# Optimization experiments

Measured on AMD Instinct MI355X. Metric: run time of the kernel, lower is better.

The kernel has to match this reference:

```python
import jax, jax.numpy as jnp
import numpy as np

EMBED = 768
HEADS = 12
HEAD_DIM = EMBED // HEADS
HIDDEN = int(EMBED * 4.0)
EPS = 1e-5


def setup_inputs() -> dict:
    key = jax.random.key(0)
    ks = jax.random.split(key, 12)
    s = 0.02
    return {
        "x": jax.random.normal(ks[0], (8, 1024, EMBED), dtype=jnp.float32),
        # norm1 / norm2 (LayerNorm affine params)
        "g1": jnp.ones((EMBED,), jnp.float32),
        "b1": jnp.zeros((EMBED,), jnp.float32),
        "g2": jnp.ones((EMBED,), jnp.float32),
        "b2": jnp.zeros((EMBED,), jnp.float32),
        # attention weights (stored [in, out]; qkv_bias=False)
        "w_qkv": jax.random.normal(ks[1], (EMBED, 3 * EMBED), jnp.float32) * s,
        "w_proj": jax.random.normal(ks[2], (EMBED, EMBED), jnp.float32) * s,
        "b_proj": jnp.zeros((EMBED,), jnp.float32),
        # MLP weights
        "w_fc1": jax.random.normal(ks[3], (EMBED, HIDDEN), jnp.float32) * s,
        "b_fc1": jnp.zeros((HIDDEN,), jnp.float32),
        "w_fc2": jax.random.normal(ks[4], (HIDDEN, EMBED), jnp.float32) * s,
        "b_fc2": jnp.zeros((EMBED,), jnp.float32),
    }


def _layernorm(x, g, b):
    mu = jnp.mean(x, axis=-1, keepdims=True)
    var = jnp.var(x, axis=-1, keepdims=True)
    return (x - mu) * jax.lax.rsqrt(var + EPS) * g + b


def reference(x, g1, b1, g2, b2, w_qkv, w_proj, b_proj, w_fc1, b_fc1, w_fc2, b_fc2):
    B, N, C = x.shape
    scaling = HEAD_DIM ** (-0.5)

    # --- attention branch ---
    h = _layernorm(x, g1, b1)
    qkv = (h @ w_qkv).reshape(B, N, 3, HEADS, HEAD_DIM)
    q, k, v = qkv[:, :, 0], qkv[:, :, 1], qkv[:, :, 2]  # [B, N, H, D]
    attn = jnp.einsum("bnhd,bmhd->bhnm", q, k) * scaling  # full NxN scores
    attn = jax.nn.softmax(attn, axis=-1)
    out = jnp.einsum("bhnm,bmhd->bnhd", attn, v).reshape(B, N, C)
    out = out @ w_proj + b_proj
    x = x + out

    # --- MLP branch ---
    h = _layernorm(x, g2, b2)
    h = jax.nn.gelu(h @ w_fc1 + b_fc1, approximate=False)
    h = h @ w_fc2 + b_fc2
    return x + h
```

## Files before the change

kernel.cpp:

```cpp
#include <hip/hip_runtime.h>
#include <hip/hip_bf16.h>
#include <math.h>

#define EMBED 768
#define HEADS 12
#define HEAD_DIM 64
#define HIDDEN 3072
#define SEQ 1024
#define BATCH 8
#define TOKENS (SEQ*BATCH)

typedef unsigned short u16;
typedef __attribute__((ext_vector_type(8))) short bf16x8;
typedef __attribute__((ext_vector_type(4))) float floatx4;
typedef __attribute__((ext_vector_type(4))) u16 u16x4;
typedef __attribute__((ext_vector_type(2))) u16 u16x2;

__device__ __forceinline__ u16 f2bf(float f){
    union { float f; unsigned u; } v; v.f = f;
    unsigned r = v.u + 0x7fffu + ((v.u >> 16) & 1u);
    return (u16)(r >> 16);
}

__device__ __forceinline__ unsigned cvt_pk_bf16(float lo, float hi){
    unsigned r;
    asm("v_cvt_pk_bf16_f32 %0, %1, %2" : "=v"(r) : "v"(lo), "v"(hi));
    return r;
}

__device__ __forceinline__ void gload16(const void* g, void* l){
    __builtin_amdgcn_global_load_lds((const __attribute__((address_space(1))) void*)g,
                                     (__attribute__((address_space(3))) void*)l, 16, 0, 0);
}

__device__ __forceinline__ float gelu_fast(float x){
    float t = 1.5957691216f * (x + 0.044715f * x * x * x);
    return x / (1.0f + __expf(-t));
}

__global__ __launch_bounds__(256) void prep_kernel(const float* __restrict__ w0, const float* __restrict__ w1,
                                   const float* __restrict__ w2, const float* __restrict__ w3,
                                   u16* __restrict__ o0, u16* __restrict__ o1,
                                   u16* __restrict__ o2, u16* __restrict__ o3,
                                   const float* __restrict__ x, const float* __restrict__ g,
                                   const float* __restrict__ bln, u16* __restrict__ lnout){
    int bb = blockIdx.x;
    int tid = threadIdx.x;
    if(bb >= 6912){
        int row  = (bb - 6912) * 4 + (tid >> 6);
        int lane = tid & 63;
        const float4* xr = (const float4*)(x + (size_t)row * EMBED);
        float4 v[3];
        float s = 0.f;
        #pragma unroll
        for(int i=0;i<3;i++){
            v[i] = xr[i*64 + lane];
            s += v[i].x + v[i].y + v[i].z + v[i].w;
        }
        #pragma unroll
        for(int o=32;o>0;o>>=1) s += __shfl_xor(s, o);
        float mu = s * (1.0f/EMBED);
        float s2 = 0.f;
        #pragma unroll
        for(int i=0;i<3;i++){
            float dx = v[i].x-mu, dy = v[i].y-mu, dz = v[i].z-mu, dw = v[i].w-mu;
            s2 += dx*dx + dy*dy + dz*dz + dw*dw;
        }
        #pragma unroll
        for(int o=32;o>0;o>>=1) s2 += __shfl_xor(s2, o);
        float rstd = rsqrtf(s2*(1.0f/EMBED) + 1e-5f);
        u16* orow = lnout + (size_t)row * EMBED;
        const float4* g4 = (const float4*)g;
        const float4* b4 = (const float4*)bln;
        #pragma unroll
        for(int i=0;i<3;i++){
            int c4 = i*64 + lane;
            float4 gv = g4[c4], bv = b4[c4];
            u16x4 pk;
            pk.x = f2bf((v[i].x-mu)*rstd*gv.x + bv.x);
            pk.y = f2bf((v[i].y-mu)*rstd*gv.y + bv.y);
            pk.z = f2bf((v[i].z-mu)*rstd*gv.z + bv.z);
            pk.w = f2bf((v[i].w-mu)*rstd*gv.w + bv.w);
            *(u16x4*)(orow + c4*4) = pk;
        }
        return;
    }
    const float* W; u16* Wt; int K, N, bx, by;
    if(bb < 1728)      { int l = bb;        W=w0; Wt=o0; K=768;  N=2304; bx=l%72; by=l/72; }
    else if(bb < 2304) { int l = bb-1728;   W=w1; Wt=o1; K=768;  N=768;  bx=l%24; by=l/24; }
    else if(bb < 4608) { int l = bb-2304;   W=w2; Wt=o2; K=768;  N=3072; bx=l%96; by=l/96; }
    else               { int l = bb-4608;   W=w3; Wt=o3; K=3072; N=768;  bx=l%24; by=l/24; }

    __shared__ float tile[32][33];
    int n0 = bx * 32, k0 = by * 32;
    int tx = tid & 31, ty = tid >> 5;
    #pragma unroll
    for(int i=0;i<32;i+=8) tile[ty+i][tx] = W[(size_t)(k0+ty+i)*N + n0+tx];
    __syncthreads();
    int kp = (tid & 15)*2, nn = tid >> 4;
    #pragma unroll
    for(int p=0;p<2;p++){
        int n = nn + p*16;
        u16x2 w2v;
        w2v.x = f2bf(tile[kp  ][n]);
        w2v.y = f2bf(tile[kp+1][n]);
        *(u16x2*)(Wt + (size_t)(n0+n)*K + k0 + kp) = w2v;
    }
}

__global__ __launch_bounds__(256) void ln_kernel(const float* __restrict__ x, const float* __restrict__ g,
                                                 const float* __restrict__ b, u16* __restrict__ out){
    int row  = blockIdx.x * 4 + (threadIdx.x >> 6);
    int lane = threadIdx.x & 63;
    const float4* xr = (const float4*)(x + (size_t)row * EMBED);
    float4 v[3];
    float s = 0.f;
    #pragma unroll
    for(int i=0;i<3;i++){
        v[i] = xr[i*64 + lane];
        s += v[i].x + v[i].y + v[i].z + v[i].w;
    }
    #pragma unroll
    for(int o=32;o>0;o>>=1) s += __shfl_xor(s, o);
    float mu = s * (1.0f/EMBED);
    float s2 = 0.f;
    #pragma unroll
    for(int i=0;i<3;i++){
        float dx = v[i].x-mu, dy = v[i].y-mu, dz = v[i].z-mu, dw = v[i].w-mu;
        s2 += dx*dx + dy*dy + dz*dz + dw*dw;
    }
    #pragma unroll
    for(int o=32;o>0;o>>=1) s2 += __shfl_xor(s2, o);
    float rstd = rsqrtf(s2*(1.0f/EMBED) + 1e-5f);
    u16* orow = out + (size_t)row * EMBED;
    const float4* g4 = (const float4*)g;
    const float4* b4 = (const float4*)b;
    #pragma unroll
    for(int i=0;i<3;i++){
        int c4 = i*64 + lane;
        float4 gv = g4[c4], bv = b4[c4];
        u16x4 pk;
        pk.x = f2bf((v[i].x-mu)*rstd*gv.x + bv.x);
        pk.y = f2bf((v[i].y-mu)*rstd*gv.y + bv.y);
        pk.z = f2bf((v[i].z-mu)*rstd*gv.z + bv.z);
        pk.w = f2bf((v[i].w-mu)*rstd*gv.w + bv.w);
        *(u16x4*)(orow + c4*4) = pk;
    }
}

template<int EPI>
__global__ __launch_bounds__(512,4) void gemm_wide(const u16* __restrict__ A, const u16* __restrict__ Bt,
        void* __restrict__ Cout, const float* __restrict__ bias, const float* __restrict__ res,
        u16* __restrict__ vt, int M, int N, int K, int ldc){
    __shared__ __align__(16) u16 As[128*64];
    __shared__ __align__(16) u16 Bs[2*256*64];
    int tid  = threadIdx.x;
    int wave = tid >> 6, lane = tid & 63;
    int quad = lane >> 4, lm = lane & 15;
    int wm = (wave >> 2) * 64;
    int wn = (wave & 3) * 64;

    int gx = gridDim.x;
    int bid = blockIdx.y * gx + blockIdx.x;
    int nwg = gx * gridDim.y;
    int cpx = nwg >> 3;
    int swz = (bid & 7) * cpx + (bid >> 3);
    int m0 = (swz / gx) * 128, n0 = (swz % gx) * 256;

    floatx4 acc[4][4];
    #pragma unroll
    for(int i=0;i<4;i++)
        #pragma unroll
        for(int j=0;j<4;j++) acc[i][j] = (floatx4){0.f,0.f,0.f,0.f};

    int srow = tid >> 3;
    int scol = ((tid & 7) ^ (srow & 7)) * 8;
    const u16* aP[2];
    const u16* bP[4];
    #pragma unroll
    for(int p=0;p<2;p++) aP[p] = A  + (size_t)(m0 + p*64 + srow) * K + scol;
    #pragma unroll
    for(int p=0;p<4;p++) bP[p] = Bt + (size_t)(n0 + p*64 + srow) * K + scol;

    int nt = K / 64;
    #pragma unroll
    for(int p=0;p<4;p++) gload16(bP[p], Bs + p*4096 + tid*8);

    for(int t=0; t<nt; ++t){
        int cur = t & 1, nxt = cur ^ 1;
        size_t k0 = (size_t)t * 64;
        #pragma unroll
        for(int p=0;p<2;p++) gload16(aP[p] + k0, As + p*4096 + tid*8);
        if(t+1 < nt){
            #pragma unroll
            for(int p=0;p<4;p++) gload16(bP[p] + k0 + 64, Bs + nxt*16384 + p*4096 + tid*8);
            asm volatile("s_waitcnt vmcnt(4)" ::: "memory");
        } else {
            asm volatile("s_waitcnt vmcnt(0)" ::: "memory");
        }
        __builtin_amdgcn_s_barrier();
        const u16* Bc = Bs + cur*16384;
        #pragma unroll
        for(int ks=0;ks<2;ks++){
            int slotoff = (((ks*4+quad) ^ (lm&7)) << 3);
            bf16x8 af[4], bfr[4];
            #pragma unroll
            for(int i=0;i<4;i++)
                af[i]  = *(const bf16x8*)(As + (wm + i*16 + lm)*64 + slotoff);
            #pragma unroll
            for(int i=0;i<4;i++)
                bfr[i] = *(const bf16x8*)(Bc + (wn + i*16 + lm)*64 + slotoff);
            #pragma unroll
            for(int mf=0;mf<4;mf++)
                #pragma unroll
                for(int nf=0;nf<4;nf++)
                    acc[mf][nf] = __builtin_amdgcn_mfma_f32_16x16x32_bf16(af[mf], bfr[nf], acc[mf][nf], 0, 0, 0);
        }
        __builtin_amdgcn_s_barrier();
    }

    if(EPI == 3 && n0 >= 1536){
        #pragma unroll
        for(int nf=0;nf<4;nf++){
            int col = n0 + wn + nf*16 + lm;
            int hh = (col - 1536) >> 6;
            int d  = col & 63;
            #pragma unroll
            for(int mf=0;mf<4;mf++){
                int row0 = m0 + wm + mf*16 + quad*4;
                int bb  = row0 >> 10;
                int key = row0 & 1023;
                u16x4 pk;
                #pragma unroll
                for(int r=0;r<4;r++) pk[r] = f2bf(acc[mf][nf][r]);
                *(u16x4*)(vt + ((size_t)(bb*HEADS+hh)*64 + d)*SEQ + key) = pk;
            }
        }
        return;
    }

    float bvv[4];
    #pragma unroll
    for(int nf=0;nf<4;nf++) bvv[nf] = bias ? bias[n0 + wn + nf*16 + lm] : 0.f;
    #pragma unroll
    for(int mf=0;mf<4;mf++){
        int row0 = m0 + wm + mf*16 + quad*4;
        #pragma unroll
        for(int r=0;r<4;r++){
            size_t rowoff = (size_t)(row0 + r) * ldc;
            #pragma unroll
            for(int nf=0;nf<4;nf++){
                int col = n0 + wn + nf*16 + lm;
                float v = acc[mf][nf][r] + bvv[nf];
                if(EPI == 1) v = gelu_fast(v);
                if(EPI == 3 && col < 768) v *= 0.18033688011112186f;
                ((u16*)Cout)[rowoff + col] = f2bf(v);
            }
        }
    }
}

template<int EPI, int BM>
__global__ __launch_bounds__(256) void gemm_bt(const u16* __restrict__ A, const u16* __restrict__ Bt,
        void* __restrict__ Cout, const float* __restrict__ bias, const float* __restrict__ res,
        u16* __restrict__ vt, int M, int N, int K, int ldc){
    constexpr int MF = BM/32;
    __shared__ __align__(16) u16 As[BM*64];
    __shared__ __align__(16) u16 Bs[2*128*64];
    int tid  = threadIdx.x;
    int wave = tid >> 6, lane = tid & 63;
    int quad = lane >> 4, lm = lane & 15;

    int gx = gridDim.x;
    int bid = blockIdx.y * gx + blockIdx.x;
    int nwg = gx * gridDim.y;
    int cpx = nwg >> 3;
    int swz = (bid & 7) * cpx + (bid >> 3);
    int m0 = (swz / gx) * BM, n0 = (swz % gx) * 128;

    int wm = (wave & 1) * (BM/2);
    int wn = (wave >> 1) * 64;

    floatx4 acc[MF][4];
    #pragma unroll
    for(int i=0;i<MF;i++)
        #pragma unroll
        for(int j=0;j<4;j++) acc[i][j] = (floatx4){0.f,0.f,0.f,0.f};

    int srow = tid >> 3;
    int scol = ((tid & 7) ^ (srow & 7)) * 8;
    const u16* aP[MF];
    const u16* bP[4];
    #pragma unroll
    for(int p=0;p<MF;p++) aP[p] = A  + (size_t)(m0 + p*32 + srow) * K + scol;
    #pragma unroll
    for(int p=0;p<4;p++)  bP[p] = Bt + (size_t)(n0 + p*32 + srow) * K + scol;

    int nt = K / 64;
    #pragma unroll
    for(int p=0;p<4;p++) gload16(bP[p], Bs + p*2048 + tid*8);

    for(int t=0; t<nt; ++t){
        int cur = t & 1, nxt = cur ^ 1;
        size_t k0 = (size_t)t * 64;
        #pragma unroll
        for(int p=0;p<MF;p++) gload16(aP[p] + k0, As + p*2048 + tid*8);
        if(t+1 < nt){
            #pragma unroll
            for(int p=0;p<4;p++) gload16(bP[p] + k0 + 64, Bs + nxt*8192 + p*2048 + tid*8);
            asm volatile("s_waitcnt vmcnt(4)" ::: "memory");
        } else {
            asm volatile("s_waitcnt vmcnt(0)" ::: "memory");
        }
        __builtin_amdgcn_s_barrier();
        const u16* Bc = Bs + cur*8192;
        #pragma unroll
        for(int ks=0;ks<2;ks++){
            int slotoff = (((ks*4+quad) ^ (lm&7)) << 3);
            bf16x8 af[MF], bfr[4];
            #pragma unroll
            for(int i=0;i<MF;i++)
                af[i]  = *(const bf16x8*)(As + (wm + i*16 + lm)*64 + slotoff);
            #pragma unroll
            for(int i=0;i<4;i++)
                bfr[i] = *(const bf16x8*)(Bc + (wn + i*16 + lm)*64 + slotoff);
            #pragma unroll
            for(int mf=0;mf<MF;mf++)
                #pragma unroll
                for(int nf=0;nf<4;nf++)
                    acc[mf][nf] = __builtin_amdgcn_mfma_f32_16x16x32_bf16(af[mf], bfr[nf], acc[mf][nf], 0, 0, 0);
        }
        __builtin_amdgcn_s_barrier();
    }

    float bvv[4];
    #pragma unroll
    for(int nf=0;nf<4;nf++) bvv[nf] = bias ? bias[n0 + wn + nf*16 + lm] : 0.f;
    #pragma unroll
    for(int mf=0;mf<MF;mf++){
        int row0 = m0 + wm + mf*16 + quad*4;
        #pragma unroll
        for(int r=0;r<4;r++){
            size_t rowoff = (size_t)(row0 + r) * ldc;
            #pragma unroll
            for(int nf=0;nf<4;nf++){
                int col = n0 + wn + nf*16 + lm;
                float v = acc[mf][nf][r] + bvv[nf];
                if(EPI == 2){
                    ((float*)Cout)[rowoff + col] = v + res[rowoff + col];
                } else {
                    ((u16*)Cout)[rowoff + col] = f2bf(v);
                }
            }
        }
    }
}

__global__ __launch_bounds__(256) void attn_kernel(const u16* __restrict__ qk, const u16* __restrict__ vt,
                                                   u16* __restrict__ out){
    int bid = blockIdx.x;
    int hb = bid % 96;
    int qt = bid / 96;
    int h = hb % HEADS, b = hb / HEADS;
    int tid = threadIdx.x;
    int wave = tid >> 6, lane = tid & 63;
    int quad = lane >> 4, lm = lane & 15;

    __shared__ __align__(16) u16 Ks[2*64*64];
    __shared__ __align__(16) u16 Vs[2*64*64];
    __shared__ __align__(16) u16 P[4*32*64];

    const u16* qbase = qk + (size_t)b * SEQ * 1536;
    const u16* vbase = vt + (size_t)(b*HEADS + h) * 64 * SEQ;
    u16* Pw = P + wave*2048;

    int q0 = qt*128 + wave*32;
    bf16x8 qf[2][2];
    #pragma unroll
    for(int qi=0;qi<2;qi++){
        const u16* qp = qbase + (size_t)(q0 + qi*16 + lm)*1536 + h*64;
        qf[qi][0] = *(const bf16x8*)(qp + quad*8);
        qf[qi][1] = *(const bf16x8*)(qp + 32 + quad*8);
    }

    float l_i[2] = {0.f, 0.f};
    floatx4 o_acc[2][4];
    #pragma unroll
    for(int qi=0;qi<2;qi++)
        #pragma unroll
        for(int nf=0;nf<4;nf++) o_acc[qi][nf] = (floatx4){0.f,0.f,0.f,0.f};

    int sr = lane >> 3;
    int sp = lane & 7;

    auto stage = [&](int kt, int buf){
        #pragma unroll
        for(int i=0;i<2;i++){
            int rr = wave*16 + i*8 + sr;
            int sw = (sp ^ (rr & 7)) * 8;
            gload16(qbase + (size_t)(kt*64 + rr)*1536 + 768 + h*64 + sw,
                    Ks + buf*4096 + (wave*16 + i*8)*64 + lane*8);
            gload16(vbase + (size_t)rr*SEQ + kt*64 + sw,
                    Vs + buf*4096 + (wave*16 + i*8)*64 + lane*8);
        }
    };

    stage(0, 0);
    __syncthreads();

    int cur = 0;
    for(int kt=0; kt<16; kt++){
        if(kt < 15) stage(kt+1, cur^1);
        const u16* Ksb = Ks + cur*4096;
        const u16* Vsb = Vs + cur*4096;

        floatx4 s[4][2];
        #pragma unroll
        for(int kf=0;kf<4;kf++){
            int krow = kf*16 + lm;
            bf16x8 k0 = *(const bf16x8*)(Ksb + krow*64 + ((quad     ^ (lm&7))*8));
            bf16x8 k1 = *(const bf16x8*)(Ksb + krow*64 + (((4+quad) ^ (lm&7))*8));
            #pragma unroll
            for(int qi=0;qi<2;qi++){
                floatx4 t = (floatx4){0.f,0.f,0.f,0.f};
                t = __builtin_amdgcn_mfma_f32_16x16x32_bf16(k0, qf[qi][0], t, 0, 0, 0);
                t = __builtin_amdgcn_mfma_f32_16x16x32_bf16(k1, qf[qi][1], t, 0, 0, 0);
                s[kf][qi] = t;
            }
        }

        #pragma unroll
        for(int qi=0;qi<2;qi++){
            float part = 0.f;
            #pragma unroll
            for(int kf=0;kf<4;kf++){
                #pragma unroll
                for(int r=0;r<4;r++){
                    float e = exp2f(s[kf][qi][r]);
                    s[kf][qi][r] = e;
                    part += e;
                }
            }
            l_i[qi] += part;
            #pragma unroll
            for(int kf=0;kf<4;kf++){
                uint2 pk2;
                pk2.x = cvt_pk_bf16(s[kf][qi][0], s[kf][qi][1]);
                pk2.y = cvt_pk_bf16(s[kf][qi][2], s[kf][qi][3]);
                int c  = kf*4 + quad;
                int cp = c ^ (2*(lm & 7));
                *(uint2*)(Pw + (qi*16 + lm)*64 + cp*4) = pk2;
            }
        }

        #pragma unroll
        for(int ks=0;ks<2;ks++){
            bf16x8 vf[4];
            #pragma unroll
            for(int nf=0;nf<4;nf++)
                vf[nf] = *(const bf16x8*)(Vsb + (nf*16+lm)*64 + (((ks*4+quad) ^ (lm&7))*8));
            #pragma unroll
            for(int qi=0;qi<2;qi++){
                int cr = (ks*8 + 2*quad) ^ (2*(lm & 7));
                bf16x8 pa = *(const bf16x8*)(Pw + (qi*16 + lm)*64 + cr*4);
                #pragma unroll
                for(int nf=0;nf<4;nf++)
                    o_acc[qi][nf] = __builtin_amdgcn_mfma_f32_16x16x32_bf16(pa, vf[nf], o_acc[qi][nf], 0, 0, 0);
            }
        }
        if(kt < 15) __syncthreads();
        cur ^= 1;
    }

    #pragma unroll
    for(int qi=0;qi<2;qi++){
        float lf = l_i[qi];
        lf += __shfl_xor(lf, 16);
        lf += __shfl_xor(lf, 32);
        float rl[4];
        #pragma unroll
        for(int r=0;r<4;r++) rl[r] = 1.0f / __shfl(lf, quad*4 + r);
        int token = b*SEQ + qt*128 + wave*32 + qi*16 + quad*4;
        #pragma unroll
        for(int r=0;r<4;r++){
            size_t rowoff = (size_t)(token + r)*EMBED + h*64;
            #pragma unroll
            for(int nf=0;nf<4;nf++){
                out[rowoff + nf*16 + lm] = f2bf(o_acc[qi][nf][r] * rl[r]);
            }
        }
    }
}

extern "C" void kernel_launch(void* const* d_in, const int* in_sizes, int n_in,
                              void* d_out, int out_size, void* d_ws, size_t ws_size,
                              hipStream_t stream) {
    const float* x      = (const float*)d_in[0];
    const float* g1     = (const float*)d_in[1];
    const float* b1     = (const float*)d_in[2];
    const float* g2     = (const float*)d_in[3];
    const float* b2     = (const float*)d_in[4];
    const float* w_qkv  = (const float*)d_in[5];
    const float* w_proj = (const float*)d_in[6];
    const float* b_proj = (const float*)d_in[7];
    const float* w_fc1  = (const float*)d_in[8];
    const float* b_fc1  = (const float*)d_in[9];
    const float* w_fc2  = (const float*)d_in[10];
    const float* b_fc2  = (const float*)d_in[11];
    float* out = (float*)d_out;

    char* ws = (char*)d_ws;
    u16*   wqkv_t  = (u16*)  (ws + 0);
    u16*   wproj_t = (u16*)  (ws + 3538944);
    u16*   wfc1_t  = (u16*)  (ws + 4718592);
    u16*   wfc2_t  = (u16*)  (ws + 9437184);
    float* x1      = (float*)(ws + 14155776);
    u16*   hbuf    = (u16*)  (ws + 39321600);
    u16*   qkbuf   = (u16*)  (ws + 51904512);
    u16*   vtbuf   = (u16*)  (ws + 77070336);
    u16*   attn_o  = (u16*)  (ws + 89653248);
    u16*   fc1_o   = qkbuf;
    u16*   h2      = hbuf;

    prep_kernel<<<8960, 256, 0, stream>>>(w_qkv, w_proj, w_fc1, w_fc2,
                                          wqkv_t, wproj_t, wfc1_t, wfc2_t,
                                          x, g1, b1, hbuf);

    gemm_wide<3><<<dim3(2304/256, TOKENS/128), 512, 0, stream>>>(hbuf, wqkv_t, qkbuf, nullptr, nullptr, vtbuf, TOKENS, 2304, 768, 1536);

    attn_kernel<<<768, 256, 0, stream>>>(qkbuf, vtbuf, attn_o);

    gemm_bt<2,64><<<dim3( 768/128, TOKENS/64), 256, 0, stream>>>(attn_o, wproj_t, x1, b_proj, x, nullptr, TOKENS, 768, 768, 768);

    ln_kernel<<<TOKENS/4, 256, 0, stream>>>(x1, g2, b2, h2);

    gemm_wide<1><<<dim3(3072/256, TOKENS/128), 512, 0, stream>>>(h2, wfc1_t, fc1_o, b_fc1, nullptr, nullptr, TOKENS, 3072, 768, 3072);

    gemm_bt<2,64><<<dim3( 768/128, TOKENS/64), 256, 0, stream>>>(fc1_o, wfc2_t, out, b_fc2, x1, nullptr, TOKENS, 768, 3072, 768);
}
```

Baseline: 323.8 us.

## Halve GEMM K-tile to 32 and double-buffer both A and B in LDS

Both GEMM kernels move from a 64-wide K tile, where only B was double-buffered, to a 32-wide K tile with A and B both double-buffered. Each thread now issues one 16-byte load per operand slice, and the LDS swizzle is reworked for 32-element rows. The aim is to overlap all global loads with MFMA work, cut LDS footprint and raise occupancy (launch bounds are adjusted). The cost is twice as many barriers and loop iterations per K, each doing less MFMA work.

Result: slower. 363.8 us (+12.4%).

```diff
diff --git a/kernel.cpp b/kernel.cpp
--- a/kernel.cpp
+++ b/kernel.cpp
@@ -149,11 +149,13 @@
 }
 
 template<int EPI>
-__global__ __launch_bounds__(512,4) void gemm_wide(const u16* __restrict__ A, const u16* __restrict__ Bt,
+__global__ __launch_bounds__(512,2) void gemm_wide(const u16* __restrict__ A, const u16* __restrict__ Bt,
         void* __restrict__ Cout, const float* __restrict__ bias, const float* __restrict__ res,
         u16* __restrict__ vt, int M, int N, int K, int ldc){
-    __shared__ __align__(16) u16 As[128*64];
-    __shared__ __align__(16) u16 Bs[2*256*64];
+    constexpr int ASZ = 128*32;
+    constexpr int BSZ = 256*32;
+    __shared__ __align__(16) u16 As[2*ASZ];
+    __shared__ __align__(16) u16 Bs[2*BSZ];
     int tid  = threadIdx.x;
     int wave = tid >> 6, lane = tid & 63;
     int quad = lane >> 4, lm = lane & 15;
@@ -173,49 +175,45 @@
         #pragma unroll
         for(int j=0;j<4;j++) acc[i][j] = (floatx4){0.f,0.f,0.f,0.f};
 
-    int srow = tid >> 3;
-    int scol = ((tid & 7) ^ (srow & 7)) * 8;
-    const u16* aP[2];
-    const u16* bP[4];
-    #pragma unroll
-    for(int p=0;p<2;p++) aP[p] = A  + (size_t)(m0 + p*64 + srow) * K + scol;
-    #pragma unroll
-    for(int p=0;p<4;p++) bP[p] = Bt + (size_t)(n0 + p*64 + srow) * K + scol;
-
-    int nt = K / 64;
-    #pragma unroll
-    for(int p=0;p<4;p++) gload16(bP[p], Bs + p*4096 + tid*8);
+    int srow = tid >> 2;
+    int scol = ((tid & 3) ^ ((tid >> 4) & 3)) * 8;
+    const u16* aP  = A  + (size_t)(m0 + srow) * K + scol;
+    const u16* bP0 = Bt + (size_t)(n0 + srow) * K + scol;
+    const u16* bP1 = Bt + (size_t)(n0 + 128 + srow) * K + scol;
+    int cr8 = (quad ^ (lm >> 2)) * 8;
+
+    int nt = K / 32;
+
+    gload16(aP,  As + tid*8);
+    gload16(bP0, Bs + tid*8);
+    gload16(bP1, Bs + 4096 + tid*8);
 
     for(int t=0; t<nt; ++t){
         int cur = t & 1, nxt = cur ^ 1;
-        size_t k0 = (size_t)t * 64;
-        #pragma unroll
-        for(int p=0;p<2;p++) gload16(aP[p] + k0, As + p*4096 + tid*8);
         if(t+1 < nt){
-            #pragma unroll
-            for(int p=0;p<4;p++) gload16(bP[p] + k0 + 64, Bs + nxt*16384 + p*4096 + tid*8);
-            asm volatile("s_waitcnt vmcnt(4)" ::: "memory");
+            size_t ko = (size_t)(t+1) * 32;
+            gload16(aP  + ko, As + nxt*ASZ + tid*8);
+            gload16(bP0 + ko, Bs + nxt*BSZ + tid*8);
+            gload16(bP1 + ko, Bs + nxt*BSZ + 4096 + tid*8);
+            asm volatile("s_waitcnt vmcnt(3)" ::: "memory");
         } else {
             asm volatile("s_waitcnt vmcnt(0)" ::: "memory");
         }
         __builtin_amdgcn_s_barrier();
-        const u16* Bc = Bs + cur*16384;
-        #pragma unroll
-        for(int ks=0;ks<2;ks++){
-            int slotoff = (((ks*4+quad) ^ (lm&7)) << 3);
-            bf16x8 af[4], bfr[4];
-            #pragma unroll
-            for(int i=0;i<4;i++)
-                af[i]  = *(const bf16x8*)(As + (wm + i*16 + lm)*64 + slotoff);
-            #pragma unroll
-            for(int i=0;i<4;i++)
-                bfr[i] = *(const bf16x8*)(Bc + (wn + i*16 + lm)*64 + slotoff);
-            #pragma unroll
-            for(int mf=0;mf<4;mf++)
-                #pragma unroll
-                for(int nf=0;nf<4;nf++)
-                    acc[mf][nf] = __builtin_amdgcn_mfma_f32_16x16x32_bf16(af[mf], bfr[nf], acc[mf][nf], 0, 0, 0);
-        }
+        const u16* Ac = As + cur*ASZ;
+        const u16* Bc = Bs + cur*BSZ;
+        bf16x8 af[4], bfr[4];
+        #pragma unroll
+        for(int mf=0;mf<4;mf++)
+            af[mf]  = *(const bf16x8*)(Ac + (wm + mf*16 + lm)*32 + cr8);
+        #pragma unroll
+        for(int nf=0;nf<4;nf++)
+            bfr[nf] = *(const bf16x8*)(Bc + (wn + nf*16 + lm)*32 + cr8);
+        #pragma unroll
+        for(int mf=0;mf<4;mf++)
+            #pragma unroll
+            for(int nf=0;nf<4;nf++)
+                acc[mf][nf] = __builtin_amdgcn_mfma_f32_16x16x32_bf16(af[mf], bfr[nf], acc[mf][nf], 0, 0, 0);
         __builtin_amdgcn_s_barrier();
     }
 
@@ -260,13 +258,14 @@
     }
 }
 
-template<int EPI, int BM>
-__global__ __launch_bounds__(256) void gemm_bt(const u16* __restrict__ A, const u16* __restrict__ Bt,
+template<int EPI>
+__global__ __launch_bounds__(256,4) void gemm_nar(const u16* __restrict__ A, const u16* __restrict__ Bt,
         void* __restrict__ Cout, const float* __restrict__ bias, const float* __restrict__ res,
         u16* __restrict__ vt, int M, int N, int K, int ldc){
-    constexpr int MF = BM/32;
-    __shared__ __align__(16) u16 As[BM*64];
-    __shared__ __align__(16) u16 Bs[2*128*64];
+    constexpr int ASZ = 64*32;
+    constexpr int BSZ = 128*32;
+    __shared__ __align__(16) u16 As[2*ASZ];
+    __shared__ __align__(16) u16 Bs[2*BSZ];
     int tid  = threadIdx.x;
     int wave = tid >> 6, lane = tid & 63;
     int quad = lane >> 4, lm = lane & 15;
@@ -276,60 +275,56 @@
     int nwg = gx * gridDim.y;
     int cpx = nwg >> 3;
     int swz = (bid & 7) * cpx + (bid >> 3);
-    int m0 = (swz / gx) * BM, n0 = (swz % gx) * 128;
-
-    int wm = (wave & 1) * (BM/2);
+    int m0 = (swz / gx) * 64, n0 = (swz % gx) * 128;
+
+    int wm = (wave & 1) * 32;
     int wn = (wave >> 1) * 64;
 
-    floatx4 acc[MF][4];
-    #pragma unroll
-    for(int i=0;i<MF;i++)
+    floatx4 acc[2][4];
+    #pragma unroll
+    for(int i=0;i<2;i++)
         #pragma unroll
         for(int j=0;j<4;j++) acc[i][j] = (floatx4){0.f,0.f,0.f,0.f};
 
-    int srow = tid >> 3;
-    int scol = ((tid & 7) ^ (srow & 7)) * 8;
-    const u16* aP[MF];
-    const u16* bP[4];
-    #pragma unroll
-    for(int p=0;p<MF;p++) aP[p] = A  + (size_t)(m0 + p*32 + srow) * K + scol;
-    #pragma unroll
-    for(int p=0;p<4;p++)  bP[p] = Bt + (size_t)(n0 + p*32 + srow) * K + scol;
-
-    int nt = K / 64;
-    #pragma unroll
-    for(int p=0;p<4;p++) gload16(bP[p], Bs + p*2048 + tid*8);
+    int srow = tid >> 2;
+    int scol = ((tid & 3) ^ ((tid >> 4) & 3)) * 8;
+    const u16* aP  = A  + (size_t)(m0 + srow) * K + scol;
+    const u16* bP0 = Bt + (size_t)(n0 + srow) * K + scol;
+    const u16* bP1 = Bt + (size_t)(n0 + 64 + srow) * K + scol;
+    int cr8 = (quad ^ (lm >> 2)) * 8;
+
+    int nt = K / 32;
+
+    gload16(aP,  As + tid*8);
+    gload16(bP0, Bs + tid*8);
+    gload16(bP1, Bs + 2048 + tid*8);
 
     for(int t=0; t<nt; ++t){
         int cur = t & 1, nxt = cur ^ 1;
-        size_t k0 = (size_t)t * 64;
-        #pragma unroll
-        for(int p=0;p<MF;p++) gload16(aP[p] + k0, As + p*2048 + tid*8);
         if(t+1 < nt){
-            #pragma unroll
-            for(int p=0;p<4;p++) gload16(bP[p] + k0 + 64, Bs + nxt*8192 + p*2048 + tid*8);
-            asm volatile("s_waitcnt vmcnt(4)" ::: "memory");
+            size_t ko = (size_t)(t+1) * 32;
+            gload16(aP  + ko, As + nxt*ASZ + tid*8);
+            gload16(bP0 + ko, Bs + nxt*BSZ + tid*8);
+            gload16(bP1 + ko, Bs + nxt*BSZ + 2048 + tid*8);
+            asm volatile("s_waitcnt vmcnt(3)" ::: "memory");
         } else {
             asm volatile("s_waitcnt vmcnt(0)" ::: "memory");
         }
         __builtin_amdgcn_s_barrier();
-        const u16* Bc = Bs + cur*8192;
-        #pragma unroll
-        for(int ks=0;ks<2;ks++){
-            int slotoff = (((ks*4+quad) ^ (lm&7)) << 3);
-            bf16x8 af[MF], bfr[4];
-            #pragma unroll
-            for(int i=0;i<MF;i++)
-                af[i]  = *(const bf16x8*)(As + (wm + i*16 + lm)*64 + slotoff);
-            #pragma unroll
-            for(int i=0;i<4;i++)
-                bfr[i] = *(const bf16x8*)(Bc + (wn + i*16 + lm)*64 + slotoff);
-            #pragma unroll
-            for(int mf=0;mf<MF;mf++)
-                #pragma unroll
-                for(int nf=0;nf<4;nf++)
-                    acc[mf][nf] = __builtin_amdgcn_mfma_f32_16x16x32_bf16(af[mf], bfr[nf], acc[mf][nf], 0, 0, 0);
-        }
+        const u16* Ac = As + cur*ASZ;
+        const u16* Bc = Bs + cur*BSZ;
+        bf16x8 af[2], bfr[4];
+        #pragma unroll
+        for(int mf=0;mf<2;mf++)
+            af[mf]  = *(const bf16x8*)(Ac + (wm + mf*16 + lm)*32 + cr8);
+        #pragma unroll
+        for(int nf=0;nf<4;nf++)
+            bfr[nf] = *(const bf16x8*)(Bc + (wn + nf*16 + lm)*32 + cr8);
+        #pragma unroll
+        for(int mf=0;mf<2;mf++)
+            #pragma unroll
+            for(int nf=0;nf<4;nf++)
+                acc[mf][nf] = __builtin_amdgcn_mfma_f32_16x16x32_bf16(af[mf], bfr[nf], acc[mf][nf], 0, 0, 0);
         __builtin_amdgcn_s_barrier();
     }
 
@@ -337,7 +332,7 @@
     #pragma unroll
     for(int nf=0;nf<4;nf++) bvv[nf] = bias ? bias[n0 + wn + nf*16 + lm] : 0.f;
     #pragma unroll
-    for(int mf=0;mf<MF;mf++){
+    for(int mf=0;mf<2;mf++){
         int row0 = m0 + wm + mf*16 + quad*4;
         #pragma unroll
         for(int r=0;r<4;r++){
@@ -530,11 +525,11 @@
 
     attn_kernel<<<768, 256, 0, stream>>>(qkbuf, vtbuf, attn_o);
 
-    gemm_bt<2,64><<<dim3( 768/128, TOKENS/64), 256, 0, stream>>>(attn_o, wproj_t, x1, b_proj, x, nullptr, TOKENS, 768, 768, 768);
+    gemm_nar<2><<<dim3( 768/128, TOKENS/64), 256, 0, stream>>>(attn_o, wproj_t, x1, b_proj, x, nullptr, TOKENS, 768, 768, 768);
 
     ln_kernel<<<TOKENS/4, 256, 0, stream>>>(x1, g2, b2, h2);
 
     gemm_wide<1><<<dim3(3072/256, TOKENS/128), 512, 0, stream>>>(h2, wfc1_t, fc1_o, b_fc1, nullptr, nullptr, TOKENS, 3072, 768, 3072);
 
-    gemm_bt<2,64><<<dim3( 768/128, TOKENS/64), 256, 0, stream>>>(fc1_o, wfc2_t, out, b_fc2, x1, nullptr, TOKENS, 768, 3072, 768);
-}
+    gemm_nar<2><<<dim3( 768/128, TOKENS/64), 256, 0, stream>>>(fc1_o, wfc2_t, out, b_fc2, x1, nullptr, TOKENS, 768, 3072, 768);
+}
```
